# Kernel optimization log

Hardware: AMD Instinct MI355X
Metric: run time of the kernel (lower is better)

## Reference

```python
import jax, jax.numpy as jnp
import numpy as np

EPS = 1e-5
COORD_TAU, COORD_KAPPA = 1.0, 1.0
COT_TAU, COT_LAM = 0.8, 0.7
GATE_FLOOR = 0.05


def _gconv(x, w, b=None):
    # grouped 1x1 conv: x [B,C,H,W], w [g, co_per_g, ci_per_g]
    B, C, H, W = x.shape
    g, co, ci = w.shape
    y = jnp.einsum('goi,bgihw->bgohw', w, x.reshape(B, g, ci, H, W)).reshape(B, g * co, H, W)
    return y if b is None else y + b[None, :, None, None]


def _conv1x1(x, w):
    # dense 1x1 conv: w [Cout, Cin]
    return jnp.einsum('oi,bihw->bohw', w, x)


def _inorm(x, g, b):
    # InstanceNorm2d(affine=True): per (B,C) stats over spatial dims, biased var
    mu = x.mean(axis=(2, 3), keepdims=True)
    var = x.var(axis=(2, 3), keepdims=True)
    return (x - mu) * jax.lax.rsqrt(var + EPS) * g[None, :, None, None] + b[None, :, None, None]


def _axis_softmax(z, L, axis):
    # stabilized softmax along a spatial axis, mean-rescaled by L
    zz = z / COORD_TAU
    zz = zz - zz.max(axis=axis, keepdims=True)
    return jax.nn.softmax(zz, axis=axis) * L


def _forward(x, compress_w, inc_g, inc_b, coord_proj_w, coord_proj_g, coord_proj_b,
             coord_h_w, coord_h_b, coord_wc_w, coord_wc_b, coord_alpha, coord_beta,
             cot_key_w, cot_val_w, cot_att1_w, cot_attn_g, cot_attn_b, cot_att2_w,
             cot_fuse_w, fusion_w, fus_g, fus_b, gate_w, expand_w):
    xc = jax.nn.relu(_inorm(_conv1x1(x, compress_w), inc_g, inc_b))  # [B,m,H,W]
    B, C, H, W = xc.shape

    # ---- Coord2H branch (use_softmax=True path) ----
    def proj(t):
        return jax.nn.silu(_inorm(_gconv(t, coord_proj_w), coord_proj_g, coord_proj_b))

    zh = _gconv(proj(xc.mean(axis=3, keepdims=True)), coord_h_w, coord_h_b)   # [B,C,H,1]
    zw = _gconv(proj(xc.mean(axis=2, keepdims=True)), coord_wc_w, coord_wc_b)  # [B,C,1,W]
    ah = _axis_softmax(zh, H, 2)
    aw = _axis_softmax(zw, W, 3)
    w_lin = coord_alpha * ah + coord_beta * aw  # broadcasts to [B,C,H,W]
    coord_out = xc * (1.0 + COORD_KAPPA * (w_lin - 1.0))

    # ---- CoT branch ----
    k1 = _gconv(xc, cot_key_w)
    v = _gconv(xc, cot_val_w)
    y = jnp.concatenate([k1, xc], axis=1)  # [B,2C,H,W]
    att = jax.nn.relu(_inorm(_gconv(y, cot_att1_w), cot_attn_g, cot_attn_b))
    att_logits = _gconv(att, cot_att2_w)
    z = (att_logits / COT_TAU).reshape(B, C, H * W)
    sm = jax.nn.softmax(z - z.max(axis=-1, keepdims=True), axis=-1).reshape(B, C, H, W) * (H * W)
    att_mix = (1.0 - COT_LAM) * jax.nn.sigmoid(att_logits) + COT_LAM * sm
    cot_out = _conv1x1(k1 + att_mix * v, cot_fuse_w)

    # ---- fusion + gate + expand ----
    fused = jax.nn.relu(_inorm(_conv1x1(jnp.concatenate([coord_out, cot_out], axis=1), fusion_w), fus_g, fus_b))
    gate = jax.nn.sigmoid(jnp.einsum('oi,bi->bo', gate_w, fused.mean(axis=(2, 3))))[:, :, None, None]  # [B,1,1,1]
    return _conv1x1(fused * (gate * (1.0 - GATE_FLOOR) + GATE_FLOOR), expand_w)


def setup_inputs() -> dict:
    key = jax.random.key(0)
    B, DIM, H, W = 8, 512, 128, 128
    RED, G = 16, 4
    m = DIM // RED  # 32
    mg = m // G     # 8
    ks = jax.random.split(key, 23)

    def n(k, s, sc=0.05):
        return jax.random.normal(k, s, dtype=jnp.float32) * sc

    return {
        'x': jax.random.normal(ks[0], (B, DIM, H, W), dtype=jnp.float32),
        'compress_w': n(ks[1], (m, DIM)),
        'inc_g': 1.0 + n(ks[2], (m,)),
        'inc_b': n(ks[3], (m,)),
        'coord_proj_w': n(ks[4], (G, mg, mg), 0.2),
        'coord_proj_g': 1.0 + n(ks[5], (m,)),
        'coord_proj_b': n(ks[6], (m,)),
        'coord_h_w': n(ks[7], (G, mg, mg), 0.2),
        'coord_h_b': n(ks[8], (m,)),
        'coord_wc_w': n(ks[9], (G, mg, mg), 0.2),
        'coord_wc_b': n(ks[10], (m,)),
        'coord_alpha': jnp.asarray(0.5, dtype=jnp.float32),
        'coord_beta': jnp.asarray(0.5, dtype=jnp.float32),
        'cot_key_w': n(ks[11], (G, mg, mg), 0.2),
        'cot_val_w': n(ks[12], (G, mg, mg), 0.2),
        'cot_att1_w': n(ks[13], (G, mg, 2 * mg), 0.2),
        'cot_attn_g': 1.0 + n(ks[14], (m,)),
        'cot_attn_b': n(ks[15], (m,)),
        'cot_att2_w': n(ks[16], (G, mg, mg), 0.2),
        'cot_fuse_w': n(ks[17], (m, m), 0.1),
        'fusion_w': n(ks[18], (m, 2 * m), 0.1),
        'fus_g': 1.0 + n(ks[19], (m,)),
        'fus_b': n(ks[20], (m,)),
        'gate_w': n(ks[21], (1, m), 0.2),
        'expand_w': n(ks[22], (DIM, m), 0.1),
    }


def reference(x, compress_w, inc_g, inc_b, coord_proj_w, coord_proj_g, coord_proj_b,
              coord_h_w, coord_h_b, coord_wc_w, coord_wc_b, coord_alpha, coord_beta,
              cot_key_w, cot_val_w, cot_att1_w, cot_attn_g, cot_attn_b, cot_att2_w,
              cot_fuse_w, fusion_w, fus_g, fus_b, gate_w, expand_w):
    return _forward(x, compress_w, inc_g, inc_b, coord_proj_w, coord_proj_g, coord_proj_b,
                    coord_h_w, coord_h_b, coord_wc_w, coord_wc_b, coord_alpha, coord_beta,
                    cot_key_w, cot_val_w, cot_att1_w, cot_attn_g, cot_attn_b, cot_att2_w,
                    cot_fuse_w, fusion_w, fus_g, fus_b, gate_w, expand_w)
```

## Files before the change

kernel.cpp:

```cpp
#include <hip/hip_runtime.h>
#include <math.h>

#define NB 8
#define CIN 512
#define CM 32
#define MG 8
#define HH 128
#define WW 128
#define HWSZ (HH*WW)
#define EPSF 1e-5f
#define COT_ITAU 1.25f
#define LAM 0.7f
#define GFLOOR 0.05f

typedef float vf4 __attribute__((ext_vector_type(4)));

__device__ __forceinline__ float wsum(float v){
#pragma unroll
  for (int o = 32; o; o >>= 1) v += __shfl_xor(v, o, 64);
  return v;
}

__device__ __forceinline__ void gload16(const float* g, float* l){
  __builtin_amdgcn_global_load_lds(
    (const __attribute__((address_space(1))) void*)g,
    (__attribute__((address_space(3))) void*)l, 16, 0, 0);
}

__global__ void k_tw(const float* __restrict__ w, float* __restrict__ wT){
  int i = blockIdx.x*256 + threadIdx.x;
  if (i < CM*CIN){
    int c = i >> 9, k = i & (CIN-1);
    wT[k*CM + c] = w[i];
  }
}

__global__ __launch_bounds__(256) void k_compress(
    const float* __restrict__ x, const float* __restrict__ wT,
    float* __restrict__ y, float* __restrict__ s1, float* __restrict__ s2)
{
  __shared__ float lds[2][CM][256];
  int tid  = threadIdx.x;
  int lane = tid & 63;
  int wv   = tid >> 6;
  int b    = blockIdx.x >> 6;
  int tile0 = (blockIdx.x & 63) << 8;
  const float* xb = x + ((size_t)b*CIN)*HWSZ + tile0;

#define STAGE(t, buf)                                                        \
  {                                                                          \
    _Pragma("unroll")                                                        \
    for (int j=0;j<8;j++){                                                   \
      int ch = wv + 4*j;                                                     \
      gload16(xb + (size_t)((t)*CM + ch)*HWSZ + lane*4, &lds[buf][ch][0]);   \
    }                                                                        \
  }

  STAGE(0, 0)
  __syncthreads();

  float acc[CM];
#pragma unroll
  for (int c=0;c<CM;c++) acc[c]=0.f;

  for (int t=0; t<16; ++t){
    int cur = t & 1;
    if (t+1 < 16) STAGE(t+1, cur^1)
    const float* wr0 = wT + t*CM*CM;
#pragma unroll
    for (int i=0;i<CM;i++){
      float xv = lds[cur][i][tid];
      const float* wr = wr0 + i*CM;
#pragma unroll
      for (int c=0;c<CM;c++) acc[c] = fmaf(wr[c], xv, acc[c]);
    }
    __syncthreads();
  }
#undef STAGE

  {
    float ms=0.f, mq=0.f;
#pragma unroll
    for (int c=0;c<CM;c++){
      float s = wsum(acc[c]);
      float q = wsum(acc[c]*acc[c]);
      if (lane==c && wv==(c>>6)){ }
      if ((tid&63)==c){ ms=s; mq=q; }
    }
    if (lane < CM){
      atomicAdd(&s1[b*CM+lane], ms);
      atomicAdd(&s2[b*CM+lane], mq);
    }
  }
#pragma unroll
  for (int c=0;c<CM;c++) lds[0][c][tid] = acc[c];
  __syncthreads();
  {
    vf4* yb = (vf4*)(y + ((size_t)b*CM)*HWSZ + tile0);
#pragma unroll
    for (int j=0;j<8;j++){
      int f = tid + 256*j;
      yb[(size_t)(f>>6)*(HWSZ/4) + (f&63)] = *((vf4*)&lds[0][f>>6][(f&63)*4]);
    }
  }
}

__global__ __launch_bounds__(256) void k_poolstat(
  const float* __restrict__ y,
  const float* __restrict__ s1i, const float* __restrict__ s2i,
  const float* __restrict__ incg, const float* __restrict__ incb,
  const float* __restrict__ kw, const float* __restrict__ a1w,
  float* __restrict__ s1, float* __restrict__ s2,
  float* __restrict__ hpool, float* __restrict__ wpart)
{
  __shared__ float nA[CM], nB[CM];
  __shared__ float sh[CM][128];
  int tid=threadIdx.x;
  int blk=blockIdx.x;
  int b = blk >> 6;
  int p = ((blk&63)<<8)+tid;
  if (tid<CM){
    float mu  = s1i[b*CM+tid]*(1.f/HWSZ);
    float var = fmaf(-mu,mu, s2i[b*CM+tid]*(1.f/HWSZ));
    float a   = rsqrtf(var+EPSF)*incg[tid];
    nA[tid]=a; nB[tid]=incb[tid]-mu*a;
  }
  __syncthreads();
  size_t base = ((size_t)b*CM)*HWSZ + p;
  float xc[CM], k1[CM], at[CM];
#pragma unroll
  for (int c=0;c<CM;c++)
    xc[c] = fmaxf(0.f, fmaf(y[base+(size_t)c*HWSZ], nA[c], nB[c]));
  if (tid>=128){
#pragma unroll
    for (int c=0;c<CM;c++) sh[c][tid-128]=xc[c];
  }
  __syncthreads();
  if (tid<128){
    float* wp = wpart + (size_t)blk*(CM*WW) + tid;
#pragma unroll
    for (int c=0;c<CM;c++) wp[c*WW] = xc[c] + sh[c][tid];
  }
  {
    int hrow = p >> 7;
    float ms=0.f;
#pragma unroll
    for (int c=0;c<CM;c++){
      float s=wsum(xc[c]);
      if ((tid&63)==c) ms=s;
    }
    int lane=tid&63;
    if (lane<CM) atomicAdd(&hpool[(b*CM+lane)*HH+hrow], ms*(1.f/WW));
  }
#pragma unroll
  for (int gI=0;gI<4;gI++)
#pragma unroll
    for (int o=0;o<MG;o++){
      float sk=0.f;
#pragma unroll
      for (int i=0;i<MG;i++) sk = fmaf(kw[gI*64+o*8+i], xc[gI*MG+i], sk);
      k1[gI*MG+o]=sk;
    }
#pragma unroll
  for (int gI=0;gI<4;gI++)
#pragma unroll
    for (int o=0;o<MG;o++){
      float s=0.f;
#pragma unroll
      for (int i=0;i<16;i++){
        float inp = (gI<2) ? k1[gI*16+i] : xc[(gI-2)*16+i];
        s = fmaf(a1w[gI*128+o*16+i], inp, s);
      }
      at[gI*MG+o]=s;
    }
  float ms=0.f,mq=0.f;
#pragma unroll
  for (int c=0;c<CM;c++){
    float s=wsum(at[c]); float q=wsum(at[c]*at[c]);
    if ((tid&63)==c){ms=s;mq=q;}
  }
  int lane=tid&63;
  if (lane<CM){ atomicAdd(&s1[b*CM+lane],ms); atomicAdd(&s2[b*CM+lane],mq); }
}

__global__ void k_wred(const float* __restrict__ wpart, float* __restrict__ wpool){
  int bc = blockIdx.x;
  int w  = threadIdx.x;
  int b  = bc >> 5;
  int c  = bc & 31;
  const float* src = wpart + (size_t)(b*64)*(CM*WW) + c*WW + w;
  float s=0.f;
#pragma unroll 8
  for (int k=0;k<64;k++) s += src[(size_t)k*(CM*WW)];
  wpool[bc*WW + w] = s*(1.0f/HH);
}

__global__ __launch_bounds__(256) void k_cot2(
  const float* __restrict__ y,
  const float* __restrict__ s1i, const float* __restrict__ s2i,
  const float* __restrict__ incg, const float* __restrict__ incb,
  const float* __restrict__ s1a, const float* __restrict__ s2a,
  const float* __restrict__ ag, const float* __restrict__ ab,
  const float* __restrict__ kw, const float* __restrict__ a1w, const float* __restrict__ a2w,
  const float* __restrict__ hpool, const float* __restrict__ wpool,
  const float* __restrict__ pjw, const float* __restrict__ pjg, const float* __restrict__ pjb,
  const float* __restrict__ chw, const float* __restrict__ chb,
  const float* __restrict__ cww, const float* __restrict__ cwb,
  float* __restrict__ es, float* __restrict__ ah, float* __restrict__ aw)
{
  __shared__ float T[CM][HH+1];
  __shared__ float sa[CM], sb[CM], smx[CM], ssc[CM];
  __shared__ float nA[CM], nB[CM], tA[CM], tB[CM];
  int tid=threadIdx.x;
  int blk=blockIdx.x;
  int b = blk >> 6;
  int p = ((blk&63)<<8)+tid;
  if (tid<CM){
    float mu  = s1i[b*CM+tid]*(1.f/HWSZ);
    float var = fmaf(-mu,mu, s2i[b*CM+tid]*(1.f/HWSZ));
    float a   = rsqrtf(var+EPSF)*incg[tid];
    nA[tid]=a; nB[tid]=incb[tid]-mu*a;
    float mu2  = s1a[b*CM+tid]*(1.f/HWSZ);
    float var2 = fmaf(-mu2,mu2, s2a[b*CM+tid]*(1.f/HWSZ));
    float a2   = rsqrtf(var2+EPSF)*ag[tid];
    tA[tid]=a2; tB[tid]=ab[tid]-mu2*a2;
  }
  __syncthreads();
  size_t base = ((size_t)b*CM)*HWSZ + p;
  float xc[CM], k1[CM], at[CM], l[CM];
#pragma unroll
  for (int c=0;c<CM;c++)
    xc[c] = fmaxf(0.f, fmaf(y[base+(size_t)c*HWSZ], nA[c], nB[c]));
#pragma unroll
  for (int gI=0;gI<4;gI++)
#pragma unroll
    for (int o=0;o<MG;o++){
      float sk=0.f;
#pragma unroll
      for (int i=0;i<MG;i++) sk = fmaf(kw[gI*64+o*8+i], xc[gI*MG+i], sk);
      k1[gI*MG+o]=sk;
    }
#pragma unroll
  for (int gI=0;gI<4;gI++)
#pragma unroll
    for (int o=0;o<MG;o++){
      float s=0.f;
#pragma unroll
      for (int i=0;i<16;i++){
        float inp = (gI<2) ? k1[gI*16+i] : xc[(gI-2)*16+i];
        s = fmaf(a1w[gI*128+o*16+i], inp, s);
      }
      at[gI*MG+o]=s;
    }
#pragma unroll
  for (int c=0;c<CM;c++)
    at[c] = fmaxf(0.f, fmaf(at[c], tA[c], tB[c]));
#pragma unroll
  for (int gI=0;gI<4;gI++)
#pragma unroll
    for (int o=0;o<MG;o++){
      float s=0.f;
#pragma unroll
      for (int i=0;i<MG;i++) s = fmaf(a2w[gI*64+o*8+i], at[gI*8+i], s);
      l[gI*MG+o]=s;
    }
  float ms=0.f;
#pragma unroll
  for (int c=0;c<CM;c++){
    float s = wsum(__expf(l[c]*COT_ITAU));
    if ((tid&63)==c) ms=s;
  }
  int lane=tid&63;
  if (lane<CM) atomicAdd(&es[b*CM+lane], ms);

  if (blk < 2*NB){
    int bb = blk>>1, path = blk&1;
    const float* pool = path ? wpool : hpool;
    const float* w2   = path ? cww : chw;
    const float* b2   = path ? cwb : chb;
    float* outp       = path ? aw  : ah;
    float z[CM];
    if (tid<HH){
      float in[CM];
#pragma unroll
      for (int c=0;c<CM;c++) in[c] = pool[(bb*CM+c)*HH + tid];
#pragma unroll
      for (int gI=0;gI<4;gI++)
#pragma unroll
        for (int o=0;o<MG;o++){
          float s=0.f;
#pragma unroll
          for (int i=0;i<MG;i++) s = fmaf(pjw[gI*64+o*8+i], in[gI*8+i], s);
          T[gI*8+o][tid] = s;
        }
    }
    __syncthreads();
    if (tid < CM){
      float s=0.f, q=0.f;
      for (int k=0;k<HH;k++){ float t=T[tid][k]; s+=t; q+=t*t; }
      float mu = s*(1.0f/HH);
      float var = q*(1.0f/HH) - mu*mu;
      float a = rsqrtf(var+EPSF)*pjg[tid];
      sa[tid]=a; sb[tid]=pjb[tid]-mu*a;
    }
    __syncthreads();
    if (tid<HH){
      float sil[CM];
#pragma unroll
      for (int c=0;c<CM;c++){
        float val = fmaf(T[c][tid], sa[c], sb[c]);
        sil[c] = val/(1.f+__expf(-val));
      }
#pragma unroll
      for (int gI=0;gI<4;gI++)
#pragma unroll
        for (int o=0;o<MG;o++){
          float s=b2[gI*8+o];
#pragma unroll
          for (int i=0;i<MG;i++) s = fmaf(w2[gI*64+o*8+i], sil[gI*8+i], s);
          z[gI*8+o]=s;
        }
    }
    __syncthreads();
    if (tid<HH){
#pragma unroll
      for (int c=0;c<CM;c++) T[c][tid]=z[c];
    }
    __syncthreads();
    if (tid < CM){
      float mx=-1e30f;
      for (int k=0;k<HH;k++) mx = fmaxf(mx, T[tid][k]);
      float s=0.f;
      for (int k=0;k<HH;k++) s += __expf(T[tid][k]-mx);
      smx[tid]=mx; ssc[tid]=(float)HH/s;
    }
    __syncthreads();
    if (tid<HH){
#pragma unroll
      for (int c=0;c<CM;c++)
        outp[(bb*CM+c)*HH + tid] = __expf(T[c][tid]-smx[c])*ssc[c];
    }
  }
}

__global__ __launch_bounds__(256) void k_mix_fuse(
  const float* __restrict__ y,
  const float* __restrict__ s1i, const float* __restrict__ s2i,
  const float* __restrict__ incg, const float* __restrict__ incb,
  const float* __restrict__ s1a, const float* __restrict__ s2a,
  const float* __restrict__ ag, const float* __restrict__ ab,
  const float* __restrict__ kw, const float* __restrict__ vw,
  const float* __restrict__ a1w, const float* __restrict__ a2w,
  const float* __restrict__ ah, const float* __restrict__ awp, const float* __restrict__ es,
  const float* __restrict__ alpha, const float* __restrict__ beta,
  const float* __restrict__ fw, const float* __restrict__ fuw,
  float* __restrict__ fpo, float* __restrict__ s1, float* __restrict__ s2)
{
  __shared__ float nA[CM], nB[CM], tA[CM], tB[CM];
  int tid=threadIdx.x;
  int b = blockIdx.x>>6;
  int p = ((blockIdx.x&63)<<8)+tid;
  int h = p >> 7, w = p & (WW-1);
  if (tid<CM){
    float mu  = s1i[b*CM+tid]*(1.f/HWSZ);
    float var = fmaf(-mu,mu, s2i[b*CM+tid]*(1.f/HWSZ));
    float a   = rsqrtf(var+EPSF)*incg[tid];
    nA[tid]=a; nB[tid]=incb[tid]-mu*a;
    float mu2  = s1a[b*CM+tid]*(1.f/HWSZ);
    float var2 = fmaf(-mu2,mu2, s2a[b*CM+tid]*(1.f/HWSZ));
    float a2   = rsqrtf(var2+EPSF)*ag[tid];
    tA[tid]=a2; tB[tid]=ab[tid]-mu2*a2;
  }
  __syncthreads();
  size_t base = ((size_t)b*CM)*HWSZ + p;
  float al=alpha[0], be=beta[0];
  float xc[CM], k1[CM], at[CM], l[CM], t[CM];
#pragma unroll
  for (int c=0;c<CM;c++)
    xc[c] = fmaxf(0.f, fmaf(y[base+(size_t)c*HWSZ], nA[c], nB[c]));
#pragma unroll
  for (int gI=0;gI<4;gI++)
#pragma unroll
    for (int o=0;o<MG;o++){
      float sk=0.f;
#pragma unroll
      for (int i=0;i<MG;i++) sk = fmaf(kw[gI*64+o*8+i], xc[gI*MG+i], sk);
      k1[gI*MG+o]=sk;
    }
#pragma unroll
  for (int gI=0;gI<4;gI++)
#pragma unroll
    for (int o=0;o<MG;o++){
      float s=0.f;
#pragma unroll
      for (int i=0;i<16;i++){
        float inp = (gI<2) ? k1[gI*16+i] : xc[(gI-2)*16+i];
        s = fmaf(a1w[gI*128+o*16+i], inp, s);
      }
      at[gI*MG+o]=s;
    }
#pragma unroll
  for (int c=0;c<CM;c++)
    at[c] = fmaxf(0.f, fmaf(at[c], tA[c], tB[c]));
#pragma unroll
  for (int gI=0;gI<4;gI++)
#pragma unroll
    for (int o=0;o<MG;o++){
      float s=0.f;
#pragma unroll
      for (int i=0;i<MG;i++) s = fmaf(a2w[gI*64+o*8+i], at[gI*8+i], s);
      l[gI*MG+o]=s;
    }
#pragma unroll
  for (int gI=0;gI<4;gI++)
#pragma unroll
    for (int o=0;o<MG;o++){
      float sv=0.f;
#pragma unroll
      for (int i=0;i<MG;i++) sv = fmaf(vw[gI*64+o*8+i], xc[gI*MG+i], sv);
      int c = gI*MG+o;
      float lgv = l[c];
      float sm = __expf(lgv*COT_ITAU) * (16384.f/es[b*CM+c]);
      float sg = 1.f/(1.f+__expf(-lgv));
      float mix = (1.f-LAM)*sg + LAM*sm;
      t[c] = fmaf(mix, sv, k1[c]);
    }
  float co[CM];
#pragma unroll
  for (int c=0;c<CM;c++){
    float wl = al*ah[(b*CM+c)*HH + h] + be*awp[(b*CM+c)*WW + w];
    co[c] = xc[c] * wl;
  }
  float cot[CM];
#pragma unroll
  for (int o=0;o<CM;o++){
    float s=0.f;
#pragma unroll
    for (int i=0;i<CM;i++) s = fmaf(fw[o*CM+i], t[i], s);
    cot[o]=s;
  }
  float ms=0.f, mq=0.f;
#pragma unroll
  for (int o=0;o<CM;o++){
    float s=0.f;
#pragma unroll
    for (int i=0;i<CM;i++) s = fmaf(fuw[o*64+i], co[i], s);
#pragma unroll
    for (int i=0;i<CM;i++) s = fmaf(fuw[o*64+32+i], cot[i], s);
    fpo[base+(size_t)o*HWSZ]=s;
    float ss = wsum(s); float qq = wsum(s*s);
    if ((tid&63)==o){ ms=ss; mq=qq; }
  }
  int lane=tid&63;
  if (lane<CM){ atomicAdd(&s1[b*CM+lane],ms); atomicAdd(&s2[b*CM+lane],mq); }
}

__global__ __launch_bounds__(256) void k_gstat(const float4* __restrict__ fp,
  const float* __restrict__ s1f, const float* __restrict__ s2f,
  const float* __restrict__ fg, const float* __restrict__ fb,
  float* __restrict__ gsum)
{
  int idx = blockIdx.x*256+threadIdx.x;
  int bc = idx >> 12;
  int c = bc & (CM-1);
  float mu  = s1f[bc]*(1.f/HWSZ);
  float var = fmaf(-mu,mu, s2f[bc]*(1.f/HWSZ));
  float a   = rsqrtf(var+EPSF)*fg[c];
  float bb  = fb[c]-mu*a;
  float4 tv = fp[idx];
  float s = fmaxf(0.f,fmaf(tv.x,a,bb))+fmaxf(0.f,fmaf(tv.y,a,bb))
          + fmaxf(0.f,fmaf(tv.z,a,bb))+fmaxf(0.f,fmaf(tv.w,a,bb));
  s = wsum(s);
  if ((threadIdx.x&63)==0) atomicAdd(&gsum[bc], s);
}

__global__ __launch_bounds__(256) void k_expand(const float4* __restrict__ fp4,
  const float* __restrict__ s1f, const float* __restrict__ s2f,
  const float* __restrict__ fg, const float* __restrict__ fb,
  const float* __restrict__ gw, const float* __restrict__ gsum,
  const float* __restrict__ ew, vf4* __restrict__ out4)
{
  __shared__ float fA[CM], fB[CM];
  int tid = threadIdx.x;
  int b = blockIdx.x >> 4;
  int tile = blockIdx.x & 15;
  int p4 = tile*256 + tid;
  int og = blockIdx.y * 64;
  if (tid<CM){
    float mu  = s1f[b*CM+tid]*(1.f/HWSZ);
    float var = fmaf(-mu,mu, s2f[b*CM+tid]*(1.f/HWSZ));
    float a   = rsqrtf(var+EPSF)*fg[tid];
    fA[tid]=a; fB[tid]=fb[tid]-mu*a;
  }
  float s=0.f;
#pragma unroll
  for (int c=0;c<CM;c++) s = fmaf(gw[c], gsum[b*CM+c], s);
  s *= (1.0f/HWSZ);
  float gt = 1.f/(1.f+__expf(-s));
  float sc = gt*(1.f-GFLOOR)+GFLOOR;
  __syncthreads();
  float4 f[CM];
  const float4* fbp = fp4 + ((size_t)b*CM)*(HWSZ/4) + p4;
#pragma unroll
  for (int c=0;c<CM;c++){
    float4 t = fbp[(size_t)c*(HWSZ/4)];
    float a=fA[c], bb=fB[c];
    f[c].x = fmaxf(0.f, fmaf(t.x,a,bb))*sc;
    f[c].y = fmaxf(0.f, fmaf(t.y,a,bb))*sc;
    f[c].z = fmaxf(0.f, fmaf(t.z,a,bb))*sc;
    f[c].w = fmaxf(0.f, fmaf(t.w,a,bb))*sc;
  }
  vf4* ob = out4 + ((size_t)b*CIN + og)*(HWSZ/4) + p4;
  for (int j=0;j<64;j++){
    const float* wr = ew + (og+j)*CM;
    vf4 acc = (vf4)(0.f);
#pragma unroll
    for (int c=0;c<CM;c++){
      float wv = wr[c];
      acc.x = fmaf(wv, f[c].x, acc.x);
      acc.y = fmaf(wv, f[c].y, acc.y);
      acc.z = fmaf(wv, f[c].z, acc.z);
      acc.w = fmaf(wv, f[c].w, acc.w);
    }
    __builtin_nontemporal_store(acc, &ob[(size_t)j*(HWSZ/4)]);
  }
}

extern "C" void kernel_launch(void* const* d_in, const int* in_sizes, int n_in,
                              void* d_out, int out_size, void* d_ws, size_t ws_size,
                              hipStream_t stream)
{
  const float* x    = (const float*)d_in[0];
  const float* cw   = (const float*)d_in[1];
  const float* incg = (const float*)d_in[2];
  const float* incb = (const float*)d_in[3];
  const float* pjw  = (const float*)d_in[4];
  const float* pjg  = (const float*)d_in[5];
  const float* pjb  = (const float*)d_in[6];
  const float* chw  = (const float*)d_in[7];
  const float* chb  = (const float*)d_in[8];
  const float* cww  = (const float*)d_in[9];
  const float* cwb  = (const float*)d_in[10];
  const float* alpha= (const float*)d_in[11];
  const float* beta = (const float*)d_in[12];
  const float* kw   = (const float*)d_in[13];
  const float* vw   = (const float*)d_in[14];
  const float* a1w  = (const float*)d_in[15];
  const float* ag   = (const float*)d_in[16];
  const float* ab   = (const float*)d_in[17];
  const float* a2w  = (const float*)d_in[18];
  const float* fw   = (const float*)d_in[19];
  const float* fuw  = (const float*)d_in[20];
  const float* fg   = (const float*)d_in[21];
  const float* fb   = (const float*)d_in[22];
  const float* gw   = (const float*)d_in[23];
  const float* ew   = (const float*)d_in[24];
  float* out = (float*)d_out;

  float* ws = (float*)d_ws;
  const size_t BIG = (size_t)NB*CM*HWSZ;
  float* y    = ws;
  float* F    = ws +   BIG;
  float* sm   = ws + 2*BIG;
  float* acc   = sm;  sm += 2048;
  float* statS = acc,      *statQ = acc+256;
  float* attS  = acc+512,  *attQ  = acc+768;
  float* esum  = acc+1024;
  float* fusS  = acc+1280, *fusQ  = acc+1536;
  float* gsum  = acc+1792;
  float* hpool = sm;  sm += NB*CM*HH;
  float* wT    = sm;  sm += CM*CIN;
  float* wpart = sm;  sm += (size_t)512*CM*WW;
  float* wpool = sm;  sm += NB*CM*WW;
  float* ahB   = sm;  sm += NB*CM*HH;
  float* awB   = sm;  sm += NB*CM*WW;

  hipMemsetAsync(acc, 0, (2048 + NB*CM*HH)*sizeof(float), stream);
  k_tw<<<64,256,0,stream>>>(cw, wT);
  k_compress<<<512,256,0,stream>>>(x, wT, y, statS, statQ);
  k_poolstat<<<512,256,0,stream>>>(y,statS,statQ,incg,incb,kw,a1w,attS,attQ,hpool,wpart);
  k_wred<<<NB*CM,128,0,stream>>>(wpart, wpool);
  k_cot2<<<512,256,0,stream>>>(y,statS,statQ,incg,incb,attS,attQ,ag,ab,kw,a1w,a2w,
                               hpool,wpool,pjw,pjg,pjb,chw,chb,cww,cwb,esum,ahB,awB);
  k_mix_fuse<<<512,256,0,stream>>>(y,statS,statQ,incg,incb,attS,attQ,ag,ab,kw,vw,a1w,a2w,
                                   ahB,awB,esum,alpha,beta,fw,fuw,F,fusS,fusQ);
  k_gstat<<<4096,256,0,stream>>>((const float4*)F,fusS,fusQ,fg,fb,gsum);
  k_expand<<<dim3(128,8),256,0,stream>>>((const float4*)F,fusS,fusQ,fg,fb,gw,gsum,ew,(vf4*)out);
}
```

Measured before the change: 375.5 us.

## Rewrite expand 1x1 conv with bf16 MFMA and LDS-staged output tiles

The final expand kernel (32→512 channel 1x1 conv) moves from scalar FMA to bf16 16x16x32 MFMA instructions. The expand weights are converted to bf16 in the setup kernel, and activations are normalised, gated and converted to bf16 in LDS. Results are transposed through LDS so the output can be written with coalesced nontemporal vector stores. The launch grid becomes 64-pixel tiles by 128 output channels. This lowers compute cost in a kernel that is likely bound by output writes, at the cost of bf16 rounding on inputs and weights.

```diff
diff --git a/kernel.cpp b/kernel.cpp
--- a/kernel.cpp
+++ b/kernel.cpp
@@ -14,11 +14,18 @@
 #define GFLOOR 0.05f
 
 typedef float vf4 __attribute__((ext_vector_type(4)));
+typedef short bf16x8 __attribute__((ext_vector_type(8)));
+typedef float f32x4 __attribute__((ext_vector_type(4)));
 
 __device__ __forceinline__ float wsum(float v){
 #pragma unroll
   for (int o = 32; o; o >>= 1) v += __shfl_xor(v, o, 64);
   return v;
+}
+
+__device__ __forceinline__ unsigned short bfc(float x){
+  unsigned u = __float_as_uint(x);
+  return (unsigned short)((u + 0x7FFFu + ((u>>16)&1u)) >> 16);
 }
 
 __device__ __forceinline__ void gload16(const float* g, float* l){
@@ -27,11 +34,13 @@
     (__attribute__((address_space(3))) void*)l, 16, 0, 0);
 }
 
-__global__ void k_tw(const float* __restrict__ w, float* __restrict__ wT){
+__global__ void k_tw(const float* __restrict__ w, float* __restrict__ wT,
+                     const float* __restrict__ ew, unsigned short* __restrict__ ewB){
   int i = blockIdx.x*256 + threadIdx.x;
   if (i < CM*CIN){
     int c = i >> 9, k = i & (CIN-1);
     wT[k*CM + c] = w[i];
+    ewB[i] = bfc(ew[i]);
   }
 }
 
@@ -84,7 +93,6 @@
     for (int c=0;c<CM;c++){
       float s = wsum(acc[c]);
       float q = wsum(acc[c]*acc[c]);
-      if (lane==c && wv==(c>>6)){ }
       if ((tid&63)==c){ ms=s; mq=q; }
     }
     if (lane < CM){
@@ -474,55 +482,87 @@
   if ((threadIdx.x&63)==0) atomicAdd(&gsum[bc], s);
 }
 
-__global__ __launch_bounds__(256) void k_expand(const float4* __restrict__ fp4,
+__global__ __launch_bounds__(256) void k_expand_mfma(
+  const float* __restrict__ F,
   const float* __restrict__ s1f, const float* __restrict__ s2f,
   const float* __restrict__ fg, const float* __restrict__ fb,
   const float* __restrict__ gw, const float* __restrict__ gsum,
-  const float* __restrict__ ew, vf4* __restrict__ out4)
+  const unsigned short* __restrict__ ewB, float* __restrict__ out)
 {
-  __shared__ float fA[CM], fB[CM];
-  int tid = threadIdx.x;
-  int b = blockIdx.x >> 4;
-  int tile = blockIdx.x & 15;
-  int p4 = tile*256 + tid;
-  int og = blockIdx.y * 64;
+  __shared__ float outT[128][68];
+  unsigned short (*fBt)[64][8] = (unsigned short(*)[64][8])&outT[0][0];
+  __shared__ float fA[CM], fB2[CM];
+  int tid  = threadIdx.x;
+  int lane = tid & 63;
+  int wv   = tid >> 6;
+  int pt   = blockIdx.x;
+  int b    = blockIdx.y;
+  int z    = blockIdx.z;
+  int p0   = pt*64;
+
   if (tid<CM){
     float mu  = s1f[b*CM+tid]*(1.f/HWSZ);
     float var = fmaf(-mu,mu, s2f[b*CM+tid]*(1.f/HWSZ));
     float a   = rsqrtf(var+EPSF)*fg[tid];
-    fA[tid]=a; fB[tid]=fb[tid]-mu*a;
-  }
-  float s=0.f;
-#pragma unroll
-  for (int c=0;c<CM;c++) s = fmaf(gw[c], gsum[b*CM+c], s);
-  s *= (1.0f/HWSZ);
-  float gt = 1.f/(1.f+__expf(-s));
-  float sc = gt*(1.f-GFLOOR)+GFLOOR;
-  __syncthreads();
-  float4 f[CM];
-  const float4* fbp = fp4 + ((size_t)b*CM)*(HWSZ/4) + p4;
-#pragma unroll
-  for (int c=0;c<CM;c++){
-    float4 t = fbp[(size_t)c*(HWSZ/4)];
-    float a=fA[c], bb=fB[c];
-    f[c].x = fmaxf(0.f, fmaf(t.x,a,bb))*sc;
-    f[c].y = fmaxf(0.f, fmaf(t.y,a,bb))*sc;
-    f[c].z = fmaxf(0.f, fmaf(t.z,a,bb))*sc;
-    f[c].w = fmaxf(0.f, fmaf(t.w,a,bb))*sc;
-  }
-  vf4* ob = out4 + ((size_t)b*CIN + og)*(HWSZ/4) + p4;
-  for (int j=0;j<64;j++){
-    const float* wr = ew + (og+j)*CM;
-    vf4 acc = (vf4)(0.f);
-#pragma unroll
-    for (int c=0;c<CM;c++){
-      float wv = wr[c];
-      acc.x = fmaf(wv, f[c].x, acc.x);
-      acc.y = fmaf(wv, f[c].y, acc.y);
-      acc.z = fmaf(wv, f[c].z, acc.z);
-      acc.w = fmaf(wv, f[c].w, acc.w);
-    }
-    __builtin_nontemporal_store(acc, &ob[(size_t)j*(HWSZ/4)]);
+    fA[tid]=a; fB2[tid]=fb[tid]-mu*a;
+  }
+  float gs=0.f;
+#pragma unroll
+  for (int c=0;c<CM;c++) gs = fmaf(gw[c], gsum[b*CM+c], gs);
+  gs *= (1.0f/HWSZ);
+  float sc = (1.f/(1.f+__expf(-gs)))*(1.f-GFLOOR)+GFLOOR;
+  __syncthreads();
+
+  {
+    int k  = tid >> 3;
+    int pb = (tid & 7) * 8;
+    const float* Fb = F + ((size_t)(b*CM + k))*HWSZ + p0 + pb;
+    float a = fA[k], bb = fB2[k];
+    int ls_hi = (k>>3)*16;
+    int j = k & 7;
+#pragma unroll
+    for (int u=0;u<8;u++){
+      int p = pb + u;
+      float v = fmaxf(0.f, fmaf(Fb[u], a, bb))*sc;
+      fBt[p>>4][ls_hi + (p&15)][j] = bfc(v);
+    }
+  }
+  __syncthreads();
+
+  int m0 = z*128 + wv*32;
+  bf16x8 a0 = *((const bf16x8*)(ewB + (size_t)(m0      + (lane&15))*CM + (lane>>4)*8));
+  bf16x8 a1 = *((const bf16x8*)(ewB + (size_t)(m0 + 16 + (lane&15))*CM + (lane>>4)*8));
+  f32x4 acc[2][4];
+#pragma unroll
+  for (int mt=0;mt<2;mt++)
+#pragma unroll
+    for (int t=0;t<4;t++) acc[mt][t] = (f32x4)(0.f);
+#pragma unroll
+  for (int t=0;t<4;t++){
+    bf16x8 bb = *((const bf16x8*)&fBt[t][lane][0]);
+    acc[0][t] = __builtin_amdgcn_mfma_f32_16x16x32_bf16(a0, bb, acc[0][t], 0,0,0);
+    acc[1][t] = __builtin_amdgcn_mfma_f32_16x16x32_bf16(a1, bb, acc[1][t], 0,0,0);
+  }
+  __syncthreads();
+
+#pragma unroll
+  for (int mt=0;mt<2;mt++)
+#pragma unroll
+    for (int t=0;t<4;t++)
+#pragma unroll
+      for (int r=0;r<4;r++)
+        outT[wv*32 + mt*16 + (lane>>4)*4 + r][t*16 + (lane&15)] = acc[mt][t][r];
+  __syncthreads();
+
+  {
+    float* ob = out + ((size_t)(b*CIN + z*128))*HWSZ + p0;
+#pragma unroll
+    for (int k2=0;k2<8;k2++){
+      int s = tid + 256*k2;
+      int row = s >> 4, c4 = (s & 15)*4;
+      vf4 v = *((vf4*)&outT[row][c4]);
+      __builtin_nontemporal_store(v, (vf4*)(ob + (size_t)row*HWSZ + c4));
+    }
   }
 }
 
@@ -570,13 +610,14 @@
   float* gsum  = acc+1792;
   float* hpool = sm;  sm += NB*CM*HH;
   float* wT    = sm;  sm += CM*CIN;
+  unsigned short* ewB = (unsigned short*)sm; sm += CM*CIN/2;
   float* wpart = sm;  sm += (size_t)512*CM*WW;
   float* wpool = sm;  sm += NB*CM*WW;
   float* ahB   = sm;  sm += NB*CM*HH;
   float* awB   = sm;  sm += NB*CM*WW;
 
   hipMemsetAsync(acc, 0, (2048 + NB*CM*HH)*sizeof(float), stream);
-  k_tw<<<64,256,0,stream>>>(cw, wT);
+  k_tw<<<64,256,0,stream>>>(cw, wT, ew, ewB);
   k_compress<<<512,256,0,stream>>>(x, wT, y, statS, statQ);
   k_poolstat<<<512,256,0,stream>>>(y,statS,statQ,incg,incb,kw,a1w,attS,attQ,hpool,wpart);
   k_wred<<<NB*CM,128,0,stream>>>(wpart, wpool);
@@ -585,5 +626,5 @@
   k_mix_fuse<<<512,256,0,stream>>>(y,statS,statQ,incg,incb,attS,attQ,ag,ab,kw,vw,a1w,a2w,
                                    ahB,awB,esum,alpha,beta,fw,fuw,F,fusS,fusQ);
   k_gstat<<<4096,256,0,stream>>>((const float4*)F,fusS,fusQ,fg,fb,gsum);
-  k_expand<<<dim3(128,8),256,0,stream>>>((const float4*)F,fusS,fusQ,fg,fb,gw,gsum,ew,(vf4*)out);
-}
+  k_expand_mfma<<<dim3(256,8,4),256,0,stream>>>(F,fusS,fusQ,fg,fb,gw,gsum,ewB,out);
+}
```

Result: faster. 353.7 us (-5.8%).
